# Performance work log

Measured on AMD Instinct MI355X. Metric: run time of the kernel, lower is better.

Reference implementation:

```python
import jax, jax.numpy as jnp
import numpy as np
import math

# ---- hyperparameters (init_kwargs) ----
D = 2              # spatial dimension
MTOT = 65          # quadrature nodes per dimension (odd)
LENGTHSCALE = 0.1  # SE kernel lengthscale
OUTPUTSCALE = 1.0  # SE kernel variance
SIGMASQ = 0.05     # observation noise variance
CG_ITERS = 30      # fixed CG iteration count (replaces tol-based early stopping)
N_TRAIN = 100000
N_TEST = 50000
TWO_PI = 2.0 * math.pi


def setup_inputs() -> dict:
    key = jax.random.key(0)
    k1, k2, k3 = jax.random.split(key, 3)
    x = jax.random.uniform(k1, (N_TRAIN, D), dtype=jnp.float32)
    y = jax.random.normal(k2, (N_TRAIN,), dtype=jnp.float32)
    x_new = jax.random.uniform(k3, (N_TEST, D), dtype=jnp.float32)
    return {"x": x, "y": y, "x_new": x_new}


def _phases(col, h, freqs, isign):
    # exp(isign * i * 2*pi*h * x * k), shape [N, K]
    return jnp.exp((1j * isign * TWO_PI) * (h * col[:, None] * freqs[None, :]).astype(jnp.float32))


def _nudft_type1(pts, c, h, freqs):
    # fk[a,b] = sum_n c_n exp(-2*pi*i*h*(k_a x_n0 + k_b x_n1)); separable tensor grid
    E0 = _phases(pts[:, 0], h, freqs, -1.0)
    E1 = _phases(pts[:, 1], h, freqs, -1.0)
    return jnp.einsum('n,na,nb->ab', c.astype(jnp.complex64), E0, E1)


def _nudft_type2(pts, fk, h, freqs):
    # f_n = sum_{a,b} fk[a,b] exp(+2*pi*i*h*(k_a x_n0 + k_b x_n1))
    E0 = _phases(pts[:, 0], h, freqs, +1.0)
    E1 = _phases(pts[:, 1], h, freqs, +1.0)
    return jnp.einsum('ab,na,nb->n', fk, E0, E1)


def _cg(A, b, iters):
    # complex Hermitian-PSD conjugate gradients, fixed iteration count
    x0 = jnp.zeros_like(b)
    r0 = b
    rs0 = jnp.real(jnp.vdot(r0, r0))

    def step(carry, _):
        xk, r, p, rs = carry
        Ap = A(p)
        alpha = rs / jnp.real(jnp.vdot(p, Ap))
        xk = xk + alpha * p
        r = r - alpha * Ap
        rs_new = jnp.real(jnp.vdot(r, r))
        p = r + (rs_new / rs) * p
        return (xk, r, p, rs_new), None

    (xk, _, _, _), _ = jax.lax.scan(step, (x0, r0, r0, rs0), None, length=iters)
    return xk


def _forward(x, y, x_new):
    m = (MTOT - 1) // 2
    # geometry / quadrature (get_xis): domain extent L, spacing h = 1/L, grid k = -m..m
    x_all = jnp.concatenate((x, x_new), axis=0)
    L = jnp.max(jnp.max(x_all, axis=0) - jnp.min(x_all, axis=0))
    L = jnp.where(L <= 1e-9, jnp.float32(1.0), L)
    h = (1.0 / L).astype(jnp.float32)
    k = (jnp.arange(MTOT) - m).astype(jnp.float32)
    xis_1d = h * k
    X0, X1 = jnp.meshgrid(xis_1d, xis_1d, indexing='ij')
    sq = X0 * X0 + X1 * X1  # [MTOT, MTOT] squared frequency norm
    # squared-exponential spectral density S(s) = sigma_f^2 (2*pi*l^2)^(d/2) exp(-2*pi^2*l^2 |s|^2)
    l2 = LENGTHSCALE * LENGTHSCALE
    spec = OUTPUTSCALE * (TWO_PI * l2) ** (D / 2) * jnp.exp((-2.0 * math.pi ** 2 * l2) * sq)
    ws = jnp.sqrt(spec * h ** D).reshape(-1).astype(jnp.complex64)  # [M]

    # rhs = ws * F^H y  (type-1 NUFFT, exact NUDFT)
    rhs = ws * _nudft_type1(x, y, h, k).reshape(-1)

    # Toeplitz convolution vector v[o] = sum_n exp(-2*pi*i*h*o.x_n), offsets -(mtot-1)..(mtot-1)
    kk = (jnp.arange(2 * MTOT - 1) - (MTOT - 1)).astype(jnp.float32)
    Ev0 = _phases(x[:, 0], h, kk, -1.0)
    Ev1 = _phases(x[:, 1], h, kk, -1.0)
    v = jnp.einsum('na,nb->ab', Ev0, Ev1)  # [2M-1, 2M-1]
    # circularly align offset 0 to index 0, precompute FFT
    v_circ = jnp.roll(v, shift=(-(MTOT - 1), -(MTOT - 1)), axis=(0, 1))
    vhat = jnp.fft.fftn(v_circ)
    s_fft = (2 * MTOT - 1, 2 * MTOT - 1)

    def toeplitz_apply(w):  # w: [MTOT, MTOT] complex
        W = jnp.fft.fftn(w, s=s_fft)
        full = jnp.fft.ifftn(vhat * W)
        return full[:MTOT, :MTOT]

    def A_mean(beta):  # (W F^H F W + sigma^2 I) beta, beta flat [M]
        wb = (ws * beta).reshape(MTOT, MTOT)
        Tw = toeplitz_apply(wb).reshape(-1)
        return ws * Tw + SIGMASQ * beta

    beta = _cg(A_mean, rhs, CG_ITERS)
    # posterior mean at test points via type-2 NUFFT
    yhat = jnp.real(_nudft_type2(x_new, (ws * beta).reshape(MTOT, MTOT), h, k))
    return yhat


def reference(x, y, x_new):
    return _forward(x, y, x_new)
```

## Files before the change

kernel.cpp:

```cpp
#include <hip/hip_runtime.h>
#include <math.h>

#define M2 4225
#define NTRAIN 100000
#define NTEST 50000
#define CGITERS 30
#define TWO_PI_D 6.283185307179586476925287
#define TPI32 6.28318530717958647692f

#define F_H 0
#define F_RS 1
#define F_PAP 2
#define F_RSN 3
#define F_WS 8
#define F_RHS 4234
#define F_X 12684
#define F_R 21134
#define F_P 29584
#define F_AP 38034
#define F_PB 46484
#define F_VF 50710
#define F_VHAT 83992
#define F_PROD 117274
#define D_T1 75278
#define D_U 108560
#define D_VPART 125330
#define D_FKPART 2271890

#define NCHUNK 128
#define PTSB2 782
#define VHALF 8385
#define VH2 16770
#define FKHALF 2145
#define FH2 4290

__device__ __forceinline__ unsigned fkey(float f){
  unsigned u = __float_as_uint(f);
  return (u & 0x80000000u) ? ~u : (u | 0x80000000u);
}
__device__ __forceinline__ float fdec(unsigned k){
  unsigned u = (k & 0x80000000u) ? (k & 0x7fffffffu) : ~k;
  return __uint_as_float(u);
}

__global__ void k_init(unsigned* mm){
  if (threadIdx.x == 0){
    mm[0] = 0xFFFFFFFFu; mm[1] = 0u; mm[2] = 0xFFFFFFFFu; mm[3] = 0u;
  }
}

__global__ void k_minmax(const float* __restrict__ x, const float* __restrict__ xn,
                         unsigned* __restrict__ mm){
  int tid = blockIdx.x * blockDim.x + threadIdx.x;
  int str = gridDim.x * blockDim.x;
  float mn0 = 1e30f, mx0 = -1e30f, mn1 = 1e30f, mx1 = -1e30f;
  const float2* a = (const float2*)x;
  for (int i = tid; i < NTRAIN; i += str){
    float2 v = a[i];
    mn0 = fminf(mn0, v.x); mx0 = fmaxf(mx0, v.x);
    mn1 = fminf(mn1, v.y); mx1 = fmaxf(mx1, v.y);
  }
  const float2* b = (const float2*)xn;
  for (int i = tid; i < NTEST; i += str){
    float2 v = b[i];
    mn0 = fminf(mn0, v.x); mx0 = fmaxf(mx0, v.x);
    mn1 = fminf(mn1, v.y); mx1 = fmaxf(mx1, v.y);
  }
  for (int off = 32; off; off >>= 1){
    mn0 = fminf(mn0, __shfl_xor(mn0, off, 64));
    mx0 = fmaxf(mx0, __shfl_xor(mx0, off, 64));
    mn1 = fminf(mn1, __shfl_xor(mn1, off, 64));
    mx1 = fmaxf(mx1, __shfl_xor(mx1, off, 64));
  }
  if ((threadIdx.x & 63) == 0){
    atomicMin(&mm[0], fkey(mn0)); atomicMax(&mm[1], fkey(mx0));
    atomicMin(&mm[2], fkey(mn1)); atomicMax(&mm[3], fkey(mx1));
  }
}

__global__ void k_setup(float* __restrict__ wsf){
  const unsigned* mm = (const unsigned*)(wsf + 4);
  float mn0 = fdec(mm[0]), mx0 = fdec(mm[1]);
  float mn1 = fdec(mm[2]), mx1 = fdec(mm[3]);
  float d0 = __fsub_rn(mx0, mn0), d1 = __fsub_rn(mx1, mn1);
  float L = fmaxf(d0, d1);
  if (L <= 1e-9f) L = 1.0f;
  float hf = __fdiv_rn(1.0f, L);
  if (threadIdx.x == 0) wsf[F_H] = hf;
  const float c0f = (float)(TWO_PI_D * 0.01);
  const float c1f = (float)(-2.0 * 9.869604401089358618834 * 0.01);
  float h2f = __fmul_rn(hf, hf);
  for (int e = threadIdx.x; e < M2; e += blockDim.x){
    int r = e / 65, c = e - r * 65;
    float xi0 = __fmul_rn(hf, (float)(r - 32));
    float xi1 = __fmul_rn(hf, (float)(c - 32));
    float sq = __fadd_rn(__fmul_rn(xi0, xi0), __fmul_rn(xi1, xi1));
    float spec = __fmul_rn(c0f, expf(__fmul_rn(c1f, sq)));
    wsf[F_WS + e] = sqrtf(__fmul_rn(spec, h2f));
  }
}

__launch_bounds__(256)
__global__ void k_v_main(const float* __restrict__ x, const float* __restrict__ wsf,
                         double* __restrict__ vpart){
  __shared__ float2 aL[16][80];
  __shared__ float2 bL[16][80];
  __shared__ float hxs[16][2];
  const float hf = wsf[F_H];
  const int tid = threadIdx.x;
  const int t0 = tid >> 4, t1 = tid & 15;
  const int colbase = blockIdx.y * 65;
  const int ncol = blockIdx.y ? 64 : 65;
  double2 acc[5][5];
  #pragma unroll
  for (int k = 0; k < 5; ++k)
    #pragma unroll
    for (int m = 0; m < 5; ++m) acc[k][m] = make_double2(0.0, 0.0);
  const int p0 = blockIdx.x * PTSB2;
  const int pend = min(p0 + PTSB2, NTRAIN);
  for (int base = p0; base < pend; base += 16){
    if (tid < 32){
      int p = tid >> 1, d = tid & 1;
      int gp = base + p;
      hxs[p][d] = (gp < pend) ? __fmul_rn(hf, x[2 * gp + d]) : 0.f;
    }
    __syncthreads();
    for (int i = tid; i < 16 * 80; i += 256){
      int p = i / 80;
      int o = i - p * 80;
      int gp = base + p;
      float2 va = make_float2(0.f, 0.f);
      float2 vb = make_float2(0.f, 0.f);
      if (gp < pend){
        if (o < 65){
          float t = __fmul_rn(hxs[p][0], (float)o);
          float sn, cs; sincosf(__fmul_rn(TPI32, t), &sn, &cs);
          va = make_float2(cs, -sn);
        }
        if (o < ncol){
          float t = __fmul_rn(hxs[p][1], (float)(colbase + o - 64));
          float sn, cs; sincosf(__fmul_rn(TPI32, t), &sn, &cs);
          vb = make_float2(cs, -sn);
        }
      }
      aL[p][o] = va;
      bL[p][o] = vb;
    }
    __syncthreads();
    #pragma unroll 1
    for (int p = 0; p < 16; ++p){
      float2 av[5], bv[5];
      #pragma unroll
      for (int k = 0; k < 5; ++k) av[k] = aL[p][t0 + 16 * k];
      #pragma unroll
      for (int m = 0; m < 5; ++m) bv[m] = bL[p][t1 + 16 * m];
      #pragma unroll
      for (int k = 0; k < 5; ++k)
        #pragma unroll
        for (int m = 0; m < 5; ++m){
          acc[k][m].x += (double)av[k].x * (double)bv[m].x - (double)av[k].y * (double)bv[m].y;
          acc[k][m].y += (double)av[k].x * (double)bv[m].y + (double)av[k].y * (double)bv[m].x;
        }
    }
    __syncthreads();
  }
  double* outp = vpart + (size_t)blockIdx.x * VH2;
  #pragma unroll
  for (int k = 0; k < 5; ++k){
    int o0 = t0 + 16 * k;
    if (o0 < 65){
      #pragma unroll
      for (int m = 0; m < 5; ++m){
        int jl = t1 + 16 * m;
        if (jl < ncol){
          int e = o0 * 129 + colbase + jl;
          outp[2 * e] = acc[k][m].x;
          outp[2 * e + 1] = acc[k][m].y;
        }
      }
    }
  }
}

__launch_bounds__(256)
__global__ void k_fk_main(const float* __restrict__ x, const float* __restrict__ y,
                          const float* __restrict__ wsf, double* __restrict__ fkpart){
  __shared__ float2 aL[16][48];
  __shared__ float2 bL[16][80];
  __shared__ float hxs[16][2];
  __shared__ float ys[16];
  const float hf = wsf[F_H];
  const int tid = threadIdx.x;
  const int t0 = tid >> 4, t1 = tid & 15;
  double2 acc[3][5];
  #pragma unroll
  for (int k = 0; k < 3; ++k)
    #pragma unroll
    for (int m = 0; m < 5; ++m) acc[k][m] = make_double2(0.0, 0.0);
  const int p0 = blockIdx.x * PTSB2;
  const int pend = min(p0 + PTSB2, NTRAIN);
  for (int base = p0; base < pend; base += 16){
    if (tid < 32){
      int p = tid >> 1, d = tid & 1;
      int gp = base + p;
      hxs[p][d] = (gp < pend) ? __fmul_rn(hf, x[2 * gp + d]) : 0.f;
    } else if (tid < 48){
      int p = tid - 32;
      int gp = base + p;
      ys[p] = (gp < pend) ? y[gp] : 0.f;
    }
    __syncthreads();
    for (int i = tid; i < 16 * 48; i += 256){
      int p = i / 48, o = i - p * 48;
      int gp = base + p;
      float2 val = make_float2(0.f, 0.f);
      if (o < 33 && gp < pend){
        float t = __fmul_rn(hxs[p][0], (float)o);
        float sn, cs; sincosf(__fmul_rn(TPI32, t), &sn, &cs);
        val = make_float2(__fmul_rn(ys[p], cs), __fmul_rn(ys[p], -sn));
      }
      aL[p][o] = val;
    }
    for (int i = tid; i < 16 * 80; i += 256){
      int p = i / 80, j = i - p * 80;
      int gp = base + p;
      float2 val = make_float2(0.f, 0.f);
      if (j < 65 && gp < pend){
        float t = __fmul_rn(hxs[p][1], (float)(j - 32));
        float sn, cs; sincosf(__fmul_rn(TPI32, t), &sn, &cs);
        val = make_float2(cs, -sn);
      }
      bL[p][j] = val;
    }
    __syncthreads();
    #pragma unroll 1
    for (int p = 0; p < 16; ++p){
      float2 av[3], bv[5];
      #pragma unroll
      for (int k = 0; k < 3; ++k) av[k] = aL[p][t0 + 16 * k];
      #pragma unroll
      for (int m = 0; m < 5; ++m) bv[m] = bL[p][t1 + 16 * m];
      #pragma unroll
      for (int k = 0; k < 3; ++k)
        #pragma unroll
        for (int m = 0; m < 5; ++m){
          acc[k][m].x += (double)av[k].x * (double)bv[m].x - (double)av[k].y * (double)bv[m].y;
          acc[k][m].y += (double)av[k].x * (double)bv[m].y + (double)av[k].y * (double)bv[m].x;
        }
    }
    __syncthreads();
  }
  double* outp = fkpart + (size_t)blockIdx.x * FH2;
  #pragma unroll
  for (int k = 0; k < 3; ++k){
    int o0 = t0 + 16 * k;
    if (o0 < 33){
      #pragma unroll
      for (int m = 0; m < 5; ++m){
        int j = t1 + 16 * m;
        if (j < 65){
          int e = o0 * 65 + j;
          outp[2 * e] = acc[k][m].x;
          outp[2 * e + 1] = acc[k][m].y;
        }
      }
    }
  }
}

__global__ void k_reduce_v(const double* __restrict__ wsd, float* __restrict__ wsf){
  int e = blockIdx.x * blockDim.x + threadIdx.x;
  if (e >= VHALF) return;
  const double* vp = wsd + D_VPART;
  double sr = 0.0, si = 0.0;
  for (int k = 0; k < NCHUNK; ++k){
    sr += vp[(size_t)k * VH2 + 2 * e];
    si += vp[(size_t)k * VH2 + 2 * e + 1];
  }
  float r32 = (float)sr, i32 = (float)si;
  int o0 = e / 129, j = e - o0 * 129;
  float2* vF = (float2*)(wsf + F_VF);
  vF[(o0 + 64) * 129 + j] = make_float2(r32, i32);
  if (o0 > 0) vF[(64 - o0) * 129 + (128 - j)] = make_float2(r32, -i32);
}

__global__ void k_reduce_fk(const double* __restrict__ wsd, float* __restrict__ wsf){
  int e = blockIdx.x * blockDim.x + threadIdx.x;
  if (e >= FKHALF) return;
  const double* fp = wsd + D_FKPART;
  double sr = 0.0, si = 0.0;
  for (int k = 0; k < NCHUNK; ++k){
    sr += fp[(size_t)k * FH2 + 2 * e];
    si += fp[(size_t)k * FH2 + 2 * e + 1];
  }
  float fr = (float)sr, fi = (float)si;
  int a = e / 65, c = e - a * 65;
  int ef = (a + 32) * 65 + c;
  float wf = wsf[F_WS + ef];
  float* rhs = wsf + F_RHS;
  rhs[2 * ef] = __fmul_rn(wf, fr);
  rhs[2 * ef + 1] = __fmul_rn(wf, fi);
  if (a > 0){
    int ef2 = (32 - a) * 65 + (64 - c);
    float wf2 = wsf[F_WS + ef2];
    rhs[2 * ef2] = __fmul_rn(wf2, fr);
    rhs[2 * ef2 + 1] = -__fmul_rn(wf2, fi);
  }
}

__launch_bounds__(192)
__global__ void k_vhat_a(const float* __restrict__ wsf, double* __restrict__ wsd){
  __shared__ double twc[129], tws[129];
  int p = blockIdx.x, t = threadIdx.x;
  if (t < 129){
    double ang = TWO_PI_D * (double)t / 129.0;
    double s, c; sincos(ang, &s, &c);
    twc[t] = c; tws[t] = s;
  }
  __syncthreads();
  if (t >= 129) return;
  const float2* vF = (const float2*)(wsf + F_VF);
  int n = t;
  int nsrc = (n + 64) % 129;
  double ar = 0.0, ai = 0.0;
  for (int m = 0; m < 129; ++m){
    float2 v = vF[((m + 64) % 129) * 129 + nsrc];
    int idx = (p * m) % 129;
    double wr = twc[idx], wi = -tws[idx];
    ar += (double)v.x * wr - (double)v.y * wi;
    ai += (double)v.x * wi + (double)v.y * wr;
  }
  double* T1 = wsd + D_T1;
  T1[(p * 129 + n) * 2] = ar;
  T1[(p * 129 + n) * 2 + 1] = ai;
}

__launch_bounds__(192)
__global__ void k_vhat_b(const double* __restrict__ wsd, float* __restrict__ wsf){
  __shared__ double twc[129], tws[129];
  __shared__ double rowr[129], rowi[129];
  int p = blockIdx.x, t = threadIdx.x;
  if (t < 129){
    double ang = TWO_PI_D * (double)t / 129.0;
    double s, c; sincos(ang, &s, &c);
    twc[t] = c; tws[t] = s;
    const double* T1 = wsd + D_T1;
    rowr[t] = T1[(p * 129 + t) * 2];
    rowi[t] = T1[(p * 129 + t) * 2 + 1];
  }
  __syncthreads();
  if (t >= 129) return;
  int q = t;
  double ar = 0.0, ai = 0.0;
  for (int n = 0; n < 129; ++n){
    int idx = (q * n) % 129;
    double wr = twc[idx], wi = -tws[idx];
    ar += rowr[n] * wr - rowi[n] * wi;
    ai += rowr[n] * wi + rowi[n] * wr;
  }
  float2* vhat = (float2*)(wsf + F_VHAT);
  vhat[p * 129 + q] = make_float2((float)ar, (float)ai);
}

__global__ void k_cg_init(float* __restrict__ wsf){
  int e = blockIdx.x * blockDim.x + threadIdx.x;
  if (e >= M2) return;
  const float2* rhs = (const float2*)(wsf + F_RHS);
  float2 b = rhs[e];
  ((float2*)(wsf + F_X))[e] = make_float2(0.f, 0.f);
  ((float2*)(wsf + F_R))[e] = b;
  ((float2*)(wsf + F_P))[e] = b;
  wsf[F_PB + e] = __fadd_rn(__fmul_rn(b.x, b.x), __fmul_rn(b.y, b.y));
}

__device__ __forceinline__ float pw_leaf(const float* d, int o, int n){
  float r0 = d[o], r1 = d[o+1], r2 = d[o+2], r3 = d[o+3];
  float r4 = d[o+4], r5 = d[o+5], r6 = d[o+6], r7 = d[o+7];
  int i = 8;
  int lim = n - (n & 7);
  for (; i < lim; i += 8){
    r0 = __fadd_rn(r0, d[o+i]);   r1 = __fadd_rn(r1, d[o+i+1]);
    r2 = __fadd_rn(r2, d[o+i+2]); r3 = __fadd_rn(r3, d[o+i+3]);
    r4 = __fadd_rn(r4, d[o+i+4]); r5 = __fadd_rn(r5, d[o+i+5]);
    r6 = __fadd_rn(r6, d[o+i+6]); r7 = __fadd_rn(r7, d[o+i+7]);
  }
  float res = __fadd_rn(__fadd_rn(__fadd_rn(r0, r1), __fadd_rn(r2, r3)),
                        __fadd_rn(__fadd_rn(r4, r5), __fadd_rn(r6, r7)));
  for (; i < n; ++i) res = __fadd_rn(res, d[o+i]);
  return res;
}

__launch_bounds__(256)
__global__ void k_pair(float* __restrict__ wsf, int mode){
  __shared__ float pb[M2];
  __shared__ float T[16];
  int tid = threadIdx.x;
  if (mode == 1 && tid == 0) wsf[F_RS] = wsf[F_RSN];
  for (int i = tid; i < M2; i += 256) pb[i] = wsf[F_PB + i];
  __syncthreads();
  if (tid < 16){
    const int tb[16] = {0,264,528,792,1056,1320,1584,1848,
                        2112,2376,2640,2904,3168,3432,3696,3960};
    int base = tb[tid];
    int sz3 = (tid == 15) ? 73 : 72;
    float L0 = pw_leaf(pb, base, 128);
    float L1 = pw_leaf(pb, base + 128, 64);
    float L2 = pw_leaf(pb, base + 192, sz3);
    T[tid] = __fadd_rn(L0, __fadd_rn(L1, L2));
  }
  __syncthreads();
  if (tid == 0){
    float s0 = __fadd_rn(__fadd_rn(T[0], T[1]), __fadd_rn(T[2], T[3]));
    float s1 = __fadd_rn(__fadd_rn(T[4], T[5]), __fadd_rn(T[6], T[7]));
    float s2 = __fadd_rn(__fadd_rn(T[8], T[9]), __fadd_rn(T[10], T[11]));
    float s3 = __fadd_rn(__fadd_rn(T[12], T[13]), __fadd_rn(T[14], T[15]));
    float tot = __fadd_rn(__fadd_rn(s0, s1), __fadd_rn(s2, s3));
    if (mode == 0){ wsf[F_RS] = tot; wsf[F_RSN] = tot; }
    else if (mode == 1) wsf[F_PAP] = tot;
    else wsf[F_RSN] = tot;
  }
}

__launch_bounds__(192)
__global__ void k_wfft_a(const float* __restrict__ wsf, double* __restrict__ wsd){
  __shared__ double twc[129], tws[129];
  int pr = blockIdx.x, t = threadIdx.x;
  if (t < 129){
    double ang = TWO_PI_D * (double)t / 129.0;
    double s, c; sincos(ang, &s, &c);
    twc[t] = c; tws[t] = s;
  }
  __syncthreads();
  if (t >= 65) return;
  const float2* P = (const float2*)(wsf + F_P);
  const float* W = wsf + F_WS;
  int n = t;
  double ar = 0.0, ai = 0.0;
  for (int m = 0; m < 65; ++m){
    int e = m * 65 + n;
    float2 p = P[e];
    float w = W[e];
    float wbr = __fmul_rn(w, p.x), wbi = __fmul_rn(w, p.y);
    int idx = (pr * m) % 129;
    double wr = twc[idx], wi = -tws[idx];
    ar += (double)wbr * wr - (double)wbi * wi;
    ai += (double)wbr * wi + (double)wbi * wr;
  }
  double* T1 = wsd + D_T1;
  T1[(pr * 65 + n) * 2] = ar;
  T1[(pr * 65 + n) * 2 + 1] = ai;
}

__launch_bounds__(192)
__global__ void k_wfft_b(const double* __restrict__ wsd, float* __restrict__ wsf){
  __shared__ double twc[129], tws[129];
  __shared__ double rowr[65], rowi[65];
  int pr = blockIdx.x, t = threadIdx.x;
  if (t < 129){
    double ang = TWO_PI_D * (double)t / 129.0;
    double s, c; sincos(ang, &s, &c);
    twc[t] = c; tws[t] = s;
  }
  if (t < 65){
    const double* T1 = wsd + D_T1;
    rowr[t] = T1[(pr * 65 + t) * 2];
    rowi[t] = T1[(pr * 65 + t) * 2 + 1];
  }
  __syncthreads();
  if (t >= 129) return;
  int q = t;
  double ar = 0.0, ai = 0.0;
  for (int n = 0; n < 65; ++n){
    int idx = (q * n) % 129;
    double wr = twc[idx], wi = -tws[idx];
    ar += rowr[n] * wr - rowi[n] * wi;
    ai += rowr[n] * wi + rowi[n] * wr;
  }
  float Wr = (float)ar, Wi = (float)ai;
  const float2* vhat = (const float2*)(wsf + F_VHAT);
  float2 v = vhat[pr * 129 + q];
  float prre = __fsub_rn(__fmul_rn(v.x, Wr), __fmul_rn(v.y, Wi));
  float prim = __fadd_rn(__fmul_rn(v.x, Wi), __fmul_rn(v.y, Wr));
  ((float2*)(wsf + F_PROD))[pr * 129 + q] = make_float2(prre, prim);
}

__launch_bounds__(192)
__global__ void k_ifft_a(const float* __restrict__ wsf, double* __restrict__ wsd){
  __shared__ double twc[129], tws[129];
  int m = blockIdx.x, t = threadIdx.x;
  if (t < 129){
    double ang = TWO_PI_D * (double)t / 129.0;
    double s, c; sincos(ang, &s, &c);
    twc[t] = c; tws[t] = s;
  }
  __syncthreads();
  if (t >= 129) return;
  const float2* prod = (const float2*)(wsf + F_PROD);
  int q = t;
  double ar = 0.0, ai = 0.0;
  for (int pr = 0; pr < 129; ++pr){
    float2 v = prod[pr * 129 + q];
    int idx = (m * pr) % 129;
    double wr = twc[idx], wi = tws[idx];
    ar += (double)v.x * wr - (double)v.y * wi;
    ai += (double)v.x * wi + (double)v.y * wr;
  }
  const double sc = 1.0 / 129.0;
  double* U = wsd + D_U;
  U[(m * 129 + q) * 2] = ar * sc;
  U[(m * 129 + q) * 2 + 1] = ai * sc;
}

__launch_bounds__(192)
__global__ void k_ifft_b(const double* __restrict__ wsd, float* __restrict__ wsf){
  __shared__ double twc[129], tws[129];
  __shared__ double rowr[129], rowi[129];
  int m = blockIdx.x, t = threadIdx.x;
  if (t < 129){
    double ang = TWO_PI_D * (double)t / 129.0;
    double s, c; sincos(ang, &s, &c);
    twc[t] = c; tws[t] = s;
    const double* U = wsd + D_U;
    rowr[t] = U[(m * 129 + t) * 2];
    rowi[t] = U[(m * 129 + t) * 2 + 1];
  }
  __syncthreads();
  if (t >= 65) return;
  int n = t;
  double ar = 0.0, ai = 0.0;
  for (int q = 0; q < 129; ++q){
    int idx = (n * q) % 129;
    double wr = twc[idx], wi = tws[idx];
    ar += rowr[q] * wr - rowi[q] * wi;
    ai += rowr[q] * wi + rowi[q] * wr;
  }
  const double sc = 1.0 / 129.0;
  float Twr = (float)(ar * sc), Twi = (float)(ai * sc);
  int e = m * 65 + n;
  float w = wsf[F_WS + e];
  float2 p = ((const float2*)(wsf + F_P))[e];
  float Apx = __fadd_rn(__fmul_rn(w, Twr), __fmul_rn(0.05f, p.x));
  float Apy = __fadd_rn(__fmul_rn(w, Twi), __fmul_rn(0.05f, p.y));
  ((float2*)(wsf + F_AP))[e] = make_float2(Apx, Apy);
  wsf[F_PB + e] = __fadd_rn(__fmul_rn(p.x, Apx), __fmul_rn(p.y, Apy));
}

__global__ void k_update1(float* __restrict__ wsf){
  int e = blockIdx.x * blockDim.x + threadIdx.x;
  if (e >= M2) return;
  float rs = wsf[F_RS], pap = wsf[F_PAP];
  float alpha = __fdiv_rn(rs, pap);
  float2* X = (float2*)(wsf + F_X);
  float2* R = (float2*)(wsf + F_R);
  const float2* P = (const float2*)(wsf + F_P);
  const float2* AP = (const float2*)(wsf + F_AP);
  float2 p = P[e], ap = AP[e], xv = X[e], rv = R[e];
  xv.x = __fadd_rn(xv.x, __fmul_rn(alpha, p.x));
  xv.y = __fadd_rn(xv.y, __fmul_rn(alpha, p.y));
  rv.x = __fsub_rn(rv.x, __fmul_rn(alpha, ap.x));
  rv.y = __fsub_rn(rv.y, __fmul_rn(alpha, ap.y));
  X[e] = xv; R[e] = rv;
  wsf[F_PB + e] = __fadd_rn(__fmul_rn(rv.x, rv.x), __fmul_rn(rv.y, rv.y));
}

__global__ void k_update2(float* __restrict__ wsf){
  int e = blockIdx.x * blockDim.x + threadIdx.x;
  if (e >= M2) return;
  float rs = wsf[F_RS], rsn = wsf[F_RSN];
  float beta = __fdiv_rn(rsn, rs);
  const float2* R = (const float2*)(wsf + F_R);
  float2* P = (float2*)(wsf + F_P);
  float2 rv = R[e], p = P[e];
  P[e] = make_float2(__fadd_rn(rv.x, __fmul_rn(beta, p.x)),
                     __fadd_rn(rv.y, __fmul_rn(beta, p.y)));
}

__launch_bounds__(256)
__global__ void k_predict(const float* __restrict__ xn, const float* __restrict__ wsf,
                          float* __restrict__ out){
  __shared__ double fbRe[M2];
  __shared__ double fbIm[M2];
  const float hf = wsf[F_H];
  const float* wsq = wsf + F_WS;
  const float2* xb = (const float2*)(wsf + F_X);
  int tid = threadIdx.x;
  for (int i = tid; i < M2; i += 256){
    float w = wsq[i]; float2 q = xb[i];
    fbRe[i] = (double)__fmul_rn(w, q.x);
    fbIm[i] = (double)__fmul_rn(w, q.y);
  }
  __syncthreads();
  int lane = tid & 63;
  int wid = (blockIdx.x * 256 + tid) >> 6;
  int nw = (gridDim.x * 256) >> 6;
  for (int n = wid; n < NTEST; n += nw){
    float hx0 = __fmul_rn(hf, xn[2 * n]);
    float hx1 = __fmul_rn(hf, xn[2 * n + 1]);
    float t0 = __fmul_rn(hx0, (float)(lane - 32));
    float s0, c0; sincosf(__fmul_rn(TPI32, t0), &s0, &c0);
    float t1 = __fmul_rn(hx1, (float)(lane - 32));
    float s1, c1; sincosf(__fmul_rn(TPI32, t1), &s1, &c1);
    float t0x = __fmul_rn(hx0, 32.0f);
    float s0x, c0x; sincosf(__fmul_rn(TPI32, t0x), &s0x, &c0x);
    float t1x = __fmul_rn(hx1, 32.0f);
    float s1x, c1x; sincosf(__fmul_rn(TPI32, t1x), &s1x, &c1x);
    double e0r = (double)c0, e0i = (double)s0;
    double e1r = (double)c1, e1i = (double)s1;
    double gr = 0.0, gi = 0.0;
    for (int a = 0; a < 64; ++a){
      double er = __shfl(e0r, a, 64);
      double ei = __shfl(e0i, a, 64);
      double fr = fbRe[a * 65 + lane];
      double fi = fbIm[a * 65 + lane];
      gr += fr * er - fi * ei;
      gi += fr * ei + fi * er;
    }
    {
      double fr = fbRe[64 * 65 + lane], fi = fbIm[64 * 65 + lane];
      gr += fr * (double)c0x - fi * (double)s0x;
      gi += fr * (double)s0x + fi * (double)c0x;
    }
    double contrib = gr * e1r - gi * e1i;
    {
      double fr = fbRe[lane * 65 + 64], fi = fbIm[lane * 65 + 64];
      double ur = fr * e0r - fi * e0i;
      double ui = fr * e0i + fi * e0r;
      contrib += ur * (double)c1x - ui * (double)s1x;
      if (lane == 0){
        double fr2 = fbRe[64 * 65 + 64], fi2 = fbIm[64 * 65 + 64];
        double vr = fr2 * (double)c0x - fi2 * (double)s0x;
        double vi = fr2 * (double)s0x + fi2 * (double)c0x;
        contrib += vr * (double)c1x - vi * (double)s1x;
      }
    }
    for (int off = 32; off; off >>= 1) contrib += __shfl_xor(contrib, off, 64);
    if (lane == 0) out[n] = (float)contrib;
  }
}

extern "C" void kernel_launch(void* const* d_in, const int* in_sizes, int n_in,
                              void* d_out, int out_size, void* d_ws, size_t ws_size,
                              hipStream_t stream){
  const float* x = (const float*)d_in[0];
  const float* y = (const float*)d_in[1];
  const float* xnew = (const float*)d_in[2];
  float* wsf = (float*)d_ws;
  double* wsd = (double*)d_ws;
  float* out = (float*)d_out;
  unsigned* mm = (unsigned*)(wsf + 4);

  k_init<<<1, 64, 0, stream>>>(mm);
  k_minmax<<<256, 256, 0, stream>>>(x, xnew, mm);
  k_setup<<<1, 256, 0, stream>>>(wsf);
  k_v_main<<<dim3(NCHUNK, 2), 256, 0, stream>>>(x, wsf, wsd + D_VPART);
  k_fk_main<<<NCHUNK, 256, 0, stream>>>(x, y, wsf, wsd + D_FKPART);
  k_reduce_v<<<33, 256, 0, stream>>>(wsd, wsf);
  k_reduce_fk<<<9, 256, 0, stream>>>(wsd, wsf);
  k_vhat_a<<<129, 192, 0, stream>>>(wsf, wsd);
  k_vhat_b<<<129, 192, 0, stream>>>(wsd, wsf);
  k_cg_init<<<17, 256, 0, stream>>>(wsf);
  k_pair<<<1, 256, 0, stream>>>(wsf, 0);
  for (int it = 0; it < CGITERS; ++it){
    k_wfft_a<<<129, 192, 0, stream>>>(wsf, wsd);
    k_wfft_b<<<129, 192, 0, stream>>>(wsd, wsf);
    k_ifft_a<<<65, 192, 0, stream>>>(wsf, wsd);
    k_ifft_b<<<65, 192, 0, stream>>>(wsd, wsf);
    k_pair<<<1, 256, 0, stream>>>(wsf, 1);
    k_update1<<<17, 256, 0, stream>>>(wsf);
    k_pair<<<1, 256, 0, stream>>>(wsf, 2);
    k_update2<<<17, 256, 0, stream>>>(wsf);
  }
  k_predict<<<256, 256, 0, stream>>>(xnew, wsf, out);
}
```

Before: 2.605 ms.

## Fuse FFT passes and CG update kernels to cut launches per iteration

Each pair of 1-D DFT passes (vhat, forward wfft, inverse ifft) is merged into one kernel that keeps the intermediate row in shared memory instead of writing it to a global double scratch buffer. The two reduction kernels and two update kernels of each CG step become one single-block kernel, so each iteration launches 3 kernels instead of 8. This removes launch overhead and global round trips. The price is that the CG update runs on a single workgroup. The dense kernels also gain a launch_bounds occupancy hint.

```diff
diff --git a/kernel.cpp b/kernel.cpp
--- a/kernel.cpp
+++ b/kernel.cpp
@@ -22,8 +22,6 @@
 #define F_VF 50710
 #define F_VHAT 83992
 #define F_PROD 117274
-#define D_T1 75278
-#define D_U 108560
 #define D_VPART 125330
 #define D_FKPART 2271890
 
@@ -100,7 +98,7 @@
   }
 }
 
-__launch_bounds__(256)
+__launch_bounds__(256, 1)
 __global__ void k_v_main(const float* __restrict__ x, const float* __restrict__ wsf,
                          double* __restrict__ vpart){
   __shared__ float2 aL[16][80];
@@ -182,7 +180,7 @@
   }
 }
 
-__launch_bounds__(256)
+__launch_bounds__(256, 1)
 __global__ void k_fk_main(const float* __restrict__ x, const float* __restrict__ y,
                           const float* __restrict__ wsf, double* __restrict__ fkpart){
   __shared__ float2 aL[16][48];
@@ -309,8 +307,9 @@
 }
 
 __launch_bounds__(192)
-__global__ void k_vhat_a(const float* __restrict__ wsf, double* __restrict__ wsd){
+__global__ void k_vhat(float* __restrict__ wsf){
   __shared__ double twc[129], tws[129];
+  __shared__ double t1r[129], t1i[129];
   int p = blockIdx.x, t = threadIdx.x;
   if (t < 129){
     double ang = TWO_PI_D * (double)t / 129.0;
@@ -318,48 +317,32 @@
     twc[t] = c; tws[t] = s;
   }
   __syncthreads();
-  if (t >= 129) return;
-  const float2* vF = (const float2*)(wsf + F_VF);
-  int n = t;
-  int nsrc = (n + 64) % 129;
-  double ar = 0.0, ai = 0.0;
-  for (int m = 0; m < 129; ++m){
-    float2 v = vF[((m + 64) % 129) * 129 + nsrc];
-    int idx = (p * m) % 129;
-    double wr = twc[idx], wi = -tws[idx];
-    ar += (double)v.x * wr - (double)v.y * wi;
-    ai += (double)v.x * wi + (double)v.y * wr;
-  }
-  double* T1 = wsd + D_T1;
-  T1[(p * 129 + n) * 2] = ar;
-  T1[(p * 129 + n) * 2 + 1] = ai;
-}
-
-__launch_bounds__(192)
-__global__ void k_vhat_b(const double* __restrict__ wsd, float* __restrict__ wsf){
-  __shared__ double twc[129], tws[129];
-  __shared__ double rowr[129], rowi[129];
-  int p = blockIdx.x, t = threadIdx.x;
   if (t < 129){
-    double ang = TWO_PI_D * (double)t / 129.0;
-    double s, c; sincos(ang, &s, &c);
-    twc[t] = c; tws[t] = s;
-    const double* T1 = wsd + D_T1;
-    rowr[t] = T1[(p * 129 + t) * 2];
-    rowi[t] = T1[(p * 129 + t) * 2 + 1];
-  }
-  __syncthreads();
-  if (t >= 129) return;
-  int q = t;
-  double ar = 0.0, ai = 0.0;
-  for (int n = 0; n < 129; ++n){
-    int idx = (q * n) % 129;
-    double wr = twc[idx], wi = -tws[idx];
-    ar += rowr[n] * wr - rowi[n] * wi;
-    ai += rowr[n] * wi + rowi[n] * wr;
-  }
-  float2* vhat = (float2*)(wsf + F_VHAT);
-  vhat[p * 129 + q] = make_float2((float)ar, (float)ai);
+    const float2* vF = (const float2*)(wsf + F_VF);
+    int n = t;
+    int nsrc = (n + 64) % 129;
+    double ar = 0.0, ai = 0.0;
+    for (int m = 0; m < 129; ++m){
+      float2 v = vF[((m + 64) % 129) * 129 + nsrc];
+      int idx = (p * m) % 129;
+      double wr = twc[idx], wi = -tws[idx];
+      ar += (double)v.x * wr - (double)v.y * wi;
+      ai += (double)v.x * wi + (double)v.y * wr;
+    }
+    t1r[n] = ar; t1i[n] = ai;
+  }
+  __syncthreads();
+  if (t < 129){
+    int q = t;
+    double ar = 0.0, ai = 0.0;
+    for (int n = 0; n < 129; ++n){
+      int idx = (q * n) % 129;
+      double wr = twc[idx], wi = -tws[idx];
+      ar += t1r[n] * wr - t1i[n] * wi;
+      ai += t1r[n] * wi + t1i[n] * wr;
+    }
+    ((float2*)(wsf + F_VHAT))[p * 129 + q] = make_float2((float)ar, (float)ai);
+  }
 }
 
 __global__ void k_cg_init(float* __restrict__ wsf){
@@ -390,14 +373,7 @@
   return res;
 }
 
-__launch_bounds__(256)
-__global__ void k_pair(float* __restrict__ wsf, int mode){
-  __shared__ float pb[M2];
-  __shared__ float T[16];
-  int tid = threadIdx.x;
-  if (mode == 1 && tid == 0) wsf[F_RS] = wsf[F_RSN];
-  for (int i = tid; i < M2; i += 256) pb[i] = wsf[F_PB + i];
-  __syncthreads();
+__device__ __forceinline__ void pw_tree(const float* pb, float* T, int tid){
   if (tid < 16){
     const int tb[16] = {0,264,528,792,1056,1320,1584,1848,
                         2112,2376,2640,2904,3168,3432,3696,3960};
@@ -414,16 +390,26 @@
     float s1 = __fadd_rn(__fadd_rn(T[4], T[5]), __fadd_rn(T[6], T[7]));
     float s2 = __fadd_rn(__fadd_rn(T[8], T[9]), __fadd_rn(T[10], T[11]));
     float s3 = __fadd_rn(__fadd_rn(T[12], T[13]), __fadd_rn(T[14], T[15]));
-    float tot = __fadd_rn(__fadd_rn(s0, s1), __fadd_rn(s2, s3));
-    if (mode == 0){ wsf[F_RS] = tot; wsf[F_RSN] = tot; }
-    else if (mode == 1) wsf[F_PAP] = tot;
-    else wsf[F_RSN] = tot;
-  }
+    T[0] = __fadd_rn(__fadd_rn(s0, s1), __fadd_rn(s2, s3));
+  }
+}
+
+__launch_bounds__(256)
+__global__ void k_pair0(float* __restrict__ wsf){
+  __shared__ float pb[M2];
+  __shared__ float T[16];
+  int tid = threadIdx.x;
+  for (int i = tid; i < M2; i += 256) pb[i] = wsf[F_PB + i];
+  __syncthreads();
+  pw_tree(pb, T, tid);
+  __syncthreads();
+  if (tid == 0) wsf[F_RS] = T[0];
 }
 
 __launch_bounds__(192)
-__global__ void k_wfft_a(const float* __restrict__ wsf, double* __restrict__ wsd){
+__global__ void k_wfft(float* __restrict__ wsf){
   __shared__ double twc[129], tws[129];
+  __shared__ double t1r[65], t1i[65];
   int pr = blockIdx.x, t = threadIdx.x;
   if (t < 129){
     double ang = TWO_PI_D * (double)t / 129.0;
@@ -431,62 +417,45 @@
     twc[t] = c; tws[t] = s;
   }
   __syncthreads();
-  if (t >= 65) return;
-  const float2* P = (const float2*)(wsf + F_P);
-  const float* W = wsf + F_WS;
-  int n = t;
-  double ar = 0.0, ai = 0.0;
-  for (int m = 0; m < 65; ++m){
-    int e = m * 65 + n;
-    float2 p = P[e];
-    float w = W[e];
-    float wbr = __fmul_rn(w, p.x), wbi = __fmul_rn(w, p.y);
-    int idx = (pr * m) % 129;
-    double wr = twc[idx], wi = -tws[idx];
-    ar += (double)wbr * wr - (double)wbi * wi;
-    ai += (double)wbr * wi + (double)wbi * wr;
-  }
-  double* T1 = wsd + D_T1;
-  T1[(pr * 65 + n) * 2] = ar;
-  T1[(pr * 65 + n) * 2 + 1] = ai;
+  if (t < 65){
+    const float2* P = (const float2*)(wsf + F_P);
+    const float* W = wsf + F_WS;
+    int n = t;
+    double ar = 0.0, ai = 0.0;
+    for (int m = 0; m < 65; ++m){
+      int e = m * 65 + n;
+      float2 p = P[e];
+      float w = W[e];
+      float wbr = __fmul_rn(w, p.x), wbi = __fmul_rn(w, p.y);
+      int idx = (pr * m) % 129;
+      double wr = twc[idx], wi = -tws[idx];
+      ar += (double)wbr * wr - (double)wbi * wi;
+      ai += (double)wbr * wi + (double)wbi * wr;
+    }
+    t1r[n] = ar; t1i[n] = ai;
+  }
+  __syncthreads();
+  if (t < 129){
+    int q = t;
+    double ar = 0.0, ai = 0.0;
+    for (int n = 0; n < 65; ++n){
+      int idx = (q * n) % 129;
+      double wr = twc[idx], wi = -tws[idx];
+      ar += t1r[n] * wr - t1i[n] * wi;
+      ai += t1r[n] * wi + t1i[n] * wr;
+    }
+    float Wr = (float)ar, Wi = (float)ai;
+    float2 v = ((const float2*)(wsf + F_VHAT))[pr * 129 + q];
+    float prre = __fsub_rn(__fmul_rn(v.x, Wr), __fmul_rn(v.y, Wi));
+    float prim = __fadd_rn(__fmul_rn(v.x, Wi), __fmul_rn(v.y, Wr));
+    ((float2*)(wsf + F_PROD))[pr * 129 + q] = make_float2(prre, prim);
+  }
 }
 
 __launch_bounds__(192)
-__global__ void k_wfft_b(const double* __restrict__ wsd, float* __restrict__ wsf){
+__global__ void k_ifft(float* __restrict__ wsf){
   __shared__ double twc[129], tws[129];
-  __shared__ double rowr[65], rowi[65];
-  int pr = blockIdx.x, t = threadIdx.x;
-  if (t < 129){
-    double ang = TWO_PI_D * (double)t / 129.0;
-    double s, c; sincos(ang, &s, &c);
-    twc[t] = c; tws[t] = s;
-  }
-  if (t < 65){
-    const double* T1 = wsd + D_T1;
-    rowr[t] = T1[(pr * 65 + t) * 2];
-    rowi[t] = T1[(pr * 65 + t) * 2 + 1];
-  }
-  __syncthreads();
-  if (t >= 129) return;
-  int q = t;
-  double ar = 0.0, ai = 0.0;
-  for (int n = 0; n < 65; ++n){
-    int idx = (q * n) % 129;
-    double wr = twc[idx], wi = -tws[idx];
-    ar += rowr[n] * wr - rowi[n] * wi;
-    ai += rowr[n] * wi + rowi[n] * wr;
-  }
-  float Wr = (float)ar, Wi = (float)ai;
-  const float2* vhat = (const float2*)(wsf + F_VHAT);
-  float2 v = vhat[pr * 129 + q];
-  float prre = __fsub_rn(__fmul_rn(v.x, Wr), __fmul_rn(v.y, Wi));
-  float prim = __fadd_rn(__fmul_rn(v.x, Wi), __fmul_rn(v.y, Wr));
-  ((float2*)(wsf + F_PROD))[pr * 129 + q] = make_float2(prre, prim);
-}
-
-__launch_bounds__(192)
-__global__ void k_ifft_a(const float* __restrict__ wsf, double* __restrict__ wsd){
-  __shared__ double twc[129], tws[129];
+  __shared__ double ur[129], ui[129];
   int m = blockIdx.x, t = threadIdx.x;
   if (t < 129){
     double ang = TWO_PI_D * (double)t / 129.0;
@@ -494,85 +463,87 @@
     twc[t] = c; tws[t] = s;
   }
   __syncthreads();
-  if (t >= 129) return;
-  const float2* prod = (const float2*)(wsf + F_PROD);
-  int q = t;
-  double ar = 0.0, ai = 0.0;
-  for (int pr = 0; pr < 129; ++pr){
-    float2 v = prod[pr * 129 + q];
-    int idx = (m * pr) % 129;
-    double wr = twc[idx], wi = tws[idx];
-    ar += (double)v.x * wr - (double)v.y * wi;
-    ai += (double)v.x * wi + (double)v.y * wr;
-  }
-  const double sc = 1.0 / 129.0;
-  double* U = wsd + D_U;
-  U[(m * 129 + q) * 2] = ar * sc;
-  U[(m * 129 + q) * 2 + 1] = ai * sc;
-}
-
-__launch_bounds__(192)
-__global__ void k_ifft_b(const double* __restrict__ wsd, float* __restrict__ wsf){
-  __shared__ double twc[129], tws[129];
-  __shared__ double rowr[129], rowi[129];
-  int m = blockIdx.x, t = threadIdx.x;
   if (t < 129){
-    double ang = TWO_PI_D * (double)t / 129.0;
-    double s, c; sincos(ang, &s, &c);
-    twc[t] = c; tws[t] = s;
-    const double* U = wsd + D_U;
-    rowr[t] = U[(m * 129 + t) * 2];
-    rowi[t] = U[(m * 129 + t) * 2 + 1];
-  }
-  __syncthreads();
-  if (t >= 65) return;
-  int n = t;
-  double ar = 0.0, ai = 0.0;
-  for (int q = 0; q < 129; ++q){
-    int idx = (n * q) % 129;
-    double wr = twc[idx], wi = tws[idx];
-    ar += rowr[q] * wr - rowi[q] * wi;
-    ai += rowr[q] * wi + rowi[q] * wr;
-  }
-  const double sc = 1.0 / 129.0;
-  float Twr = (float)(ar * sc), Twi = (float)(ai * sc);
-  int e = m * 65 + n;
-  float w = wsf[F_WS + e];
-  float2 p = ((const float2*)(wsf + F_P))[e];
-  float Apx = __fadd_rn(__fmul_rn(w, Twr), __fmul_rn(0.05f, p.x));
-  float Apy = __fadd_rn(__fmul_rn(w, Twi), __fmul_rn(0.05f, p.y));
-  ((float2*)(wsf + F_AP))[e] = make_float2(Apx, Apy);
-  wsf[F_PB + e] = __fadd_rn(__fmul_rn(p.x, Apx), __fmul_rn(p.y, Apy));
-}
-
-__global__ void k_update1(float* __restrict__ wsf){
-  int e = blockIdx.x * blockDim.x + threadIdx.x;
-  if (e >= M2) return;
-  float rs = wsf[F_RS], pap = wsf[F_PAP];
-  float alpha = __fdiv_rn(rs, pap);
+    const float2* prod = (const float2*)(wsf + F_PROD);
+    int q = t;
+    double ar = 0.0, ai = 0.0;
+    for (int pr = 0; pr < 129; ++pr){
+      float2 v = prod[pr * 129 + q];
+      int idx = (m * pr) % 129;
+      double wr = twc[idx], wi = tws[idx];
+      ar += (double)v.x * wr - (double)v.y * wi;
+      ai += (double)v.x * wi + (double)v.y * wr;
+    }
+    const double sc = 1.0 / 129.0;
+    ur[q] = ar * sc; ui[q] = ai * sc;
+  }
+  __syncthreads();
+  if (t < 65){
+    int n = t;
+    double ar = 0.0, ai = 0.0;
+    for (int q = 0; q < 129; ++q){
+      int idx = (n * q) % 129;
+      double wr = twc[idx], wi = tws[idx];
+      ar += ur[q] * wr - ui[q] * wi;
+      ai += ur[q] * wi + ui[q] * wr;
+    }
+    const double sc = 1.0 / 129.0;
+    float Twr = (float)(ar * sc), Twi = (float)(ai * sc);
+    int e = m * 65 + n;
+    float w = wsf[F_WS + e];
+    float2 p = ((const float2*)(wsf + F_P))[e];
+    float Apx = __fadd_rn(__fmul_rn(w, Twr), __fmul_rn(0.05f, p.x));
+    float Apy = __fadd_rn(__fmul_rn(w, Twi), __fmul_rn(0.05f, p.y));
+    ((float2*)(wsf + F_AP))[e] = make_float2(Apx, Apy);
+    wsf[F_PB + e] = __fadd_rn(__fmul_rn(p.x, Apx), __fmul_rn(p.y, Apy));
+  }
+}
+
+__launch_bounds__(256)
+__global__ void k_cgstep(float* __restrict__ wsf){
+  __shared__ float pb[M2];
+  __shared__ float T[16];
+  __shared__ float sh[2];
+  int tid = threadIdx.x;
+  for (int i = tid; i < M2; i += 256) pb[i] = wsf[F_PB + i];
+  __syncthreads();
+  pw_tree(pb, T, tid);
+  __syncthreads();
+  if (tid == 0){
+    float rs = wsf[F_RS];
+    sh[1] = rs;
+    sh[0] = __fdiv_rn(rs, T[0]);
+  }
+  __syncthreads();
+  float alpha = sh[0];
   float2* X = (float2*)(wsf + F_X);
   float2* R = (float2*)(wsf + F_R);
-  const float2* P = (const float2*)(wsf + F_P);
+  float2* P = (float2*)(wsf + F_P);
   const float2* AP = (const float2*)(wsf + F_AP);
-  float2 p = P[e], ap = AP[e], xv = X[e], rv = R[e];
-  xv.x = __fadd_rn(xv.x, __fmul_rn(alpha, p.x));
-  xv.y = __fadd_rn(xv.y, __fmul_rn(alpha, p.y));
-  rv.x = __fsub_rn(rv.x, __fmul_rn(alpha, ap.x));
-  rv.y = __fsub_rn(rv.y, __fmul_rn(alpha, ap.y));
-  X[e] = xv; R[e] = rv;
-  wsf[F_PB + e] = __fadd_rn(__fmul_rn(rv.x, rv.x), __fmul_rn(rv.y, rv.y));
-}
-
-__global__ void k_update2(float* __restrict__ wsf){
-  int e = blockIdx.x * blockDim.x + threadIdx.x;
-  if (e >= M2) return;
-  float rs = wsf[F_RS], rsn = wsf[F_RSN];
-  float beta = __fdiv_rn(rsn, rs);
-  const float2* R = (const float2*)(wsf + F_R);
-  float2* P = (float2*)(wsf + F_P);
-  float2 rv = R[e], p = P[e];
-  P[e] = make_float2(__fadd_rn(rv.x, __fmul_rn(beta, p.x)),
-                     __fadd_rn(rv.y, __fmul_rn(beta, p.y)));
+  for (int e = tid; e < M2; e += 256){
+    float2 p = P[e], ap = AP[e], xv = X[e], rv = R[e];
+    xv.x = __fadd_rn(xv.x, __fmul_rn(alpha, p.x));
+    xv.y = __fadd_rn(xv.y, __fmul_rn(alpha, p.y));
+    rv.x = __fsub_rn(rv.x, __fmul_rn(alpha, ap.x));
+    rv.y = __fsub_rn(rv.y, __fmul_rn(alpha, ap.y));
+    X[e] = xv; R[e] = rv;
+    pb[e] = __fadd_rn(__fmul_rn(rv.x, rv.x), __fmul_rn(rv.y, rv.y));
+  }
+  __syncthreads();
+  pw_tree(pb, T, tid);
+  __syncthreads();
+  if (tid == 0){
+    float rsn = T[0];
+    sh[0] = __fdiv_rn(rsn, sh[1]);
+    wsf[F_RS] = rsn;
+  }
+  __syncthreads();
+  float beta = sh[0];
+  for (int e = tid; e < M2; e += 256){
+    float2 rv = R[e], p = P[e];
+    P[e] = make_float2(__fadd_rn(rv.x, __fmul_rn(beta, p.x)),
+                       __fadd_rn(rv.y, __fmul_rn(beta, p.y)));
+  }
 }
 
 __launch_bounds__(256)
@@ -656,19 +627,13 @@
   k_fk_main<<<NCHUNK, 256, 0, stream>>>(x, y, wsf, wsd + D_FKPART);
   k_reduce_v<<<33, 256, 0, stream>>>(wsd, wsf);
   k_reduce_fk<<<9, 256, 0, stream>>>(wsd, wsf);
-  k_vhat_a<<<129, 192, 0, stream>>>(wsf, wsd);
-  k_vhat_b<<<129, 192, 0, stream>>>(wsd, wsf);
+  k_vhat<<<129, 192, 0, stream>>>(wsf);
   k_cg_init<<<17, 256, 0, stream>>>(wsf);
-  k_pair<<<1, 256, 0, stream>>>(wsf, 0);
+  k_pair0<<<1, 256, 0, stream>>>(wsf);
   for (int it = 0; it < CGITERS; ++it){
-    k_wfft_a<<<129, 192, 0, stream>>>(wsf, wsd);
-    k_wfft_b<<<129, 192, 0, stream>>>(wsd, wsf);
-    k_ifft_a<<<65, 192, 0, stream>>>(wsf, wsd);
-    k_ifft_b<<<65, 192, 0, stream>>>(wsd, wsf);
-    k_pair<<<1, 256, 0, stream>>>(wsf, 1);
-    k_update1<<<17, 256, 0, stream>>>(wsf);
-    k_pair<<<1, 256, 0, stream>>>(wsf, 2);
-    k_update2<<<17, 256, 0, stream>>>(wsf);
+    k_wfft<<<129, 192, 0, stream>>>(wsf);
+    k_ifft<<<65, 192, 0, stream>>>(wsf);
+    k_cgstep<<<1, 256, 0, stream>>>(wsf);
   }
   k_predict<<<256, 256, 0, stream>>>(xnew, wsf, out);
 }
```

Measured after the change: 2.426 ms. 1.07x faster.
